# Performance work log

Measured on AMD Instinct MI355X. Metric: run time of the kernel, lower is better.

## Reference

```python
import jax, jax.numpy as jnp
import numpy as np

N = 100000      # nodes
E = 1600000     # edges (before self-loops)
IN_C = 128
HID = 256
L = 4
EPS = 1e-5


def setup_inputs() -> dict:
    key = jax.random.key(0)
    ks = jax.random.split(key, 12)
    s = 0.05
    x = jax.random.normal(ks[0], (N, IN_C), dtype=jnp.float32)
    edge_index = jax.random.randint(ks[1], (2, E), 0, N, dtype=jnp.int64)
    enc_w = jax.random.normal(ks[2], (IN_C, HID), dtype=jnp.float32) * s
    enc_b = jnp.zeros((HID,), jnp.float32)
    conv_w = jax.random.normal(ks[3], (L, HID, HID), dtype=jnp.float32) * s
    conv_b = jnp.zeros((L, HID), jnp.float32)
    ln_g = jnp.ones((L, HID), jnp.float32)
    ln_b = jnp.zeros((L, HID), jnp.float32)
    lin1_w = jax.random.normal(ks[4], (HID, HID // 2), dtype=jnp.float32) * s
    lin1_b = jnp.zeros((HID // 2,), jnp.float32)
    lin2_w = jax.random.normal(ks[5], (HID // 2, 1), dtype=jnp.float32) * s
    lin2_b = jnp.zeros((1,), jnp.float32)
    return dict(x=x, edge_index=edge_index, enc_w=enc_w, enc_b=enc_b,
                conv_w=conv_w, conv_b=conv_b, ln_g=ln_g, ln_b=ln_b,
                lin1_w=lin1_w, lin1_b=lin1_b, lin2_w=lin2_w, lin2_b=lin2_b)


def _layer_norm(h, g, b):
    mu = jnp.mean(h, axis=-1, keepdims=True)
    var = jnp.mean(jnp.square(h - mu), axis=-1, keepdims=True)
    return (h - mu) * jax.lax.rsqrt(var + EPS) * g + b


def reference(x, edge_index, enc_w, enc_b, conv_w, conv_b, ln_g, ln_b,
              lin1_w, lin1_b, lin2_w, lin2_b):
    loops = jnp.arange(N, dtype=edge_index.dtype)
    row = jnp.concatenate([edge_index[0], loops])   # source
    col = jnp.concatenate([edge_index[1], loops])   # target
    # GCN symmetric norm with self-loop weight 1 (improved=False)
    deg = jax.ops.segment_sum(jnp.ones(row.shape[0], jnp.float32), col,
                              num_segments=N)
    dis = jnp.where(deg > 0, jax.lax.rsqrt(deg), 0.0)  # deg^-1/2, [N]

    h = x @ enc_w + enc_b
    for i in range(L):
        hw = h @ conv_w[i]
        # norm_e = dis[row]*dis[col]: scale at source, aggregate, scale at target
        agg = jax.ops.segment_sum((hw * dis[:, None])[row], col,
                                  num_segments=N)
        h = agg * dis[:, None] + conv_b[i]
        h = jax.nn.relu(_layer_norm(h, ln_g[i], ln_b[i]))
        # dropout p=0.1 is identity in eval mode
    h = jax.nn.relu(h @ lin1_w + lin1_b)
    return h @ lin2_w + lin2_b  # [N, 1]
```

## Files before the change

kernel.cpp:

```cpp
#include <hip/hip_runtime.h>

#define N_NODES 100000
#define N_EDGES 1600000
#define IN_C    128
#define HID     256
#define NLAYER  4

#define NBUCK 391
#define BCAP  8192
#define EPB   4096
#define CAPL  6144

typedef __attribute__((ext_vector_type(8))) __bf16 bf16x8;
typedef __attribute__((ext_vector_type(4))) float  floatx4;

__device__ inline unsigned short f2b(float f) {
    unsigned u = __builtin_bit_cast(unsigned, f);
    return (unsigned short)((u + 0x7fffu + ((u >> 16) & 1u)) >> 16);
}
__device__ inline void acc8(float* a, uint4 v) {
    unsigned wds[4] = {v.x, v.y, v.z, v.w};
    #pragma unroll
    for (int k = 0; k < 4; ++k) {
        a[2*k]   += __builtin_bit_cast(float, wds[k] << 16);
        a[2*k+1] += __builtin_bit_cast(float, wds[k] & 0xffff0000u);
    }
}
__device__ inline void gl16(const void* g, void* l) {
    __builtin_amdgcn_global_load_lds(
        (const __attribute__((address_space(1))) unsigned int*)g,
        (__attribute__((address_space(3))) unsigned int*)l, 16, 0, 0);
}

__global__ __launch_bounds__(256) void kb_scatter(
        const int* __restrict__ row, const int* __restrict__ col,
        int* __restrict__ gfill, uint2* __restrict__ pairs, int e) {
    __shared__ uint2 ep[EPB];
    __shared__ int hist[NBUCK];
    __shared__ int lbase[NBUCK];
    const int tid  = threadIdx.x;
    const int base = blockIdx.x * EPB;
    for (int b = tid; b < NBUCK; b += 256) hist[b] = 0;
    __syncthreads();
    #pragma unroll
    for (int k = 0; k < EPB / 256; ++k) {
        int i = base + k * 256 + tid;
        uint2 pr = make_uint2(0xffffffffu, 0u);
        if (i < e) {
            pr.x = (unsigned)col[i];
            pr.y = (unsigned)row[i];
            atomicAdd(&hist[pr.x >> 8], 1);
        }
        ep[k * 256 + tid] = pr;
    }
    __syncthreads();
    for (int b = tid; b < NBUCK; b += 256) {
        int h = hist[b];
        lbase[b] = h ? atomicAdd(&gfill[b], h) : 0;
    }
    __syncthreads();
    for (int b = tid; b < NBUCK; b += 256) hist[b] = 0;
    __syncthreads();
    #pragma unroll
    for (int k = 0; k < EPB / 256; ++k) {
        uint2 pr = ep[k * 256 + tid];
        if (pr.x != 0xffffffffu) {
            int bk = pr.x >> 8;
            int p  = lbase[bk] + atomicAdd(&hist[bk], 1);
            if (p < BCAP) pairs[(size_t)bk * BCAP + p] = pr;
        }
    }
}

__global__ void kb_scan(const int* __restrict__ gfill, int* __restrict__ boff,
                        int* __restrict__ offs) {
    __shared__ int wsum[8];
    const int t = threadIdx.x, lane = t & 63, w = t >> 6;
    int v = (t < NBUCK) ? gfill[t] : 0;
    int inc = v;
    #pragma unroll
    for (int o = 1; o < 64; o <<= 1) { int u = __shfl_up(inc, o); if (lane >= o) inc += u; }
    if (lane == 63) wsum[w] = inc;
    __syncthreads();
    if (t == 0) { int r = 0; for (int i = 0; i < 8; ++i) { int x = wsum[i]; wsum[i] = r; r += x; } }
    __syncthreads();
    int excl = wsum[w] + inc - v;
    if (t <= NBUCK) boff[t] = excl;
    if (t == 0) offs[N_NODES] = N_EDGES;
}

__global__ __launch_bounds__(256) void kb_build(
        const uint2* __restrict__ pairs, const int* __restrict__ gfill,
        const int* __restrict__ boff,
        int* __restrict__ offs, float* __restrict__ dis,
        int* __restrict__ srcl, int n) {
    __shared__ int lcnt[256];
    __shared__ int lstart[256];
    __shared__ int wsum[4];
    __shared__ int sl[CAPL];
    const int b = blockIdx.x;
    const int tid = threadIdx.x, lane = tid & 63, w = tid >> 6;
    int cnt = gfill[b]; if (cnt > CAPL) cnt = CAPL;
    const int base = boff[b];
    const uint2* bp = pairs + (size_t)b * BCAP;
    lcnt[tid] = 0;
    __syncthreads();
    for (int i = tid; i < cnt; i += 256)
        atomicAdd(&lcnt[bp[i].x & 255], 1);
    __syncthreads();
    int v = lcnt[tid];
    int inc = v;
    #pragma unroll
    for (int o = 1; o < 64; o <<= 1) { int u = __shfl_up(inc, o); if (lane >= o) inc += u; }
    if (lane == 63) wsum[w] = inc;
    __syncthreads();
    if (tid == 0) { int r = 0; for (int i = 0; i < 4; ++i) { int x = wsum[i]; wsum[i] = r; r += x; } }
    __syncthreads();
    int excl = wsum[w] + inc - v;
    lstart[tid] = excl;
    int node = (b << 8) + tid;
    if (node < n) {
        dis[node]  = rsqrtf((float)(v + 1));
        offs[node] = base + excl;
    }
    __syncthreads();
    lcnt[tid] = 0;
    __syncthreads();
    for (int i = tid; i < cnt; i += 256) {
        uint2 pr = bp[i];
        int c = pr.x & 255;
        int q = lstart[c] + atomicAdd(&lcnt[c], 1);
        sl[q] = (int)pr.y;
    }
    __syncthreads();
    for (int i = tid; i < cnt; i += 256)
        srcl[base + i] = sl[i];
}

__global__ void k_wtz(const float* __restrict__ enc_w, const float* __restrict__ conv_w,
                      const float* __restrict__ w1,
                      unsigned short* __restrict__ enc_t, unsigned short* __restrict__ conv_t,
                      unsigned short* __restrict__ lin1_t, int* __restrict__ gfill) {
    int idx = blockIdx.x * blockDim.x + threadIdx.x;
    if (idx < NBUCK) gfill[idx] = 0;
    if (idx < IN_C * HID) {
        int k = idx / HID, n = idx % HID;
        enc_t[n * IN_C + k] = f2b(enc_w[idx]);
    } else if (idx < IN_C * HID + NLAYER * HID * HID) {
        int r = idx - IN_C * HID;
        int l = r / (HID * HID);
        int e = r % (HID * HID);
        int k = e / HID, n = e % HID;
        conv_t[(size_t)l * HID * HID + n * HID + k] = f2b(conv_w[r]);
    } else if (idx < IN_C * HID + NLAYER * HID * HID + HID * (HID / 2)) {
        int e = idx - (IN_C * HID + NLAYER * HID * HID);
        int k = e / (HID / 2), n = e % (HID / 2);
        lin1_t[n * HID + k] = f2b(w1[e]);
    }
}

__global__ __launch_bounds__(256) void k_mme(
        const float* __restrict__ Af,
        const unsigned short* __restrict__ Wt,
        const float* __restrict__ bias,
        unsigned short* __restrict__ Cout, int M) {
    const int K = IN_C, Nn = HID;
    __shared__ unsigned short As[128 * 32];
    __shared__ unsigned short Bs[128 * 32];
    const int tid  = threadIdx.x;
    const int lane = tid & 63;
    const int w    = tid >> 6;
    const int bm   = blockIdx.x * 128;
    const int bn   = blockIdx.y * 128;

    const int i0 = tid, i1 = tid + 256;
    const int r0 = i0 >> 2, r1 = i1 >> 2;
    const int q0 = i0 & 3,  q1 = i1 & 3;
    const int a_off0 = min(bm + r0, M - 1) * K + q0 * 8;
    const int a_off1 = min(bm + r1, M - 1) * K + q1 * 8;
    const int b_off0 = (bn + r0) * K + q0 * 8;
    const int b_off1 = (bn + r1) * K + q1 * 8;

    floatx4 acc[4][4];
    #pragma unroll
    for (int i = 0; i < 4; ++i)
        #pragma unroll
        for (int j = 0; j < 4; ++j)
            acc[i][j] = (floatx4){0.f, 0.f, 0.f, 0.f};

    const int wm = (w & 1) * 64;
    const int wn = (w >> 1) * 64;
    const int fm = lane & 15;
    const int fq = (lane >> 4) * 8;

    uint4 ra0, ra1, rb0, rb1;
    auto loadA = [&](int koff, uint4& oa0, uint4& oa1) {
        float4 f0 = *(const float4*)(Af + a_off0 + koff);
        float4 f1 = *(const float4*)(Af + a_off0 + koff + 4);
        oa0.x = (unsigned)f2b(f0.x) | ((unsigned)f2b(f0.y) << 16);
        oa0.y = (unsigned)f2b(f0.z) | ((unsigned)f2b(f0.w) << 16);
        oa0.z = (unsigned)f2b(f1.x) | ((unsigned)f2b(f1.y) << 16);
        oa0.w = (unsigned)f2b(f1.z) | ((unsigned)f2b(f1.w) << 16);
        float4 g0 = *(const float4*)(Af + a_off1 + koff);
        float4 g1 = *(const float4*)(Af + a_off1 + koff + 4);
        oa1.x = (unsigned)f2b(g0.x) | ((unsigned)f2b(g0.y) << 16);
        oa1.y = (unsigned)f2b(g0.z) | ((unsigned)f2b(g0.w) << 16);
        oa1.z = (unsigned)f2b(g1.x) | ((unsigned)f2b(g1.y) << 16);
        oa1.w = (unsigned)f2b(g1.z) | ((unsigned)f2b(g1.w) << 16);
    };

    loadA(0, ra0, ra1);
    rb0 = *(const uint4*)(Wt + b_off0);
    rb1 = *(const uint4*)(Wt + b_off1);

    const int KT = K >> 5;
    for (int kt = 0; kt < KT; ++kt) {
        ((uint4*)As)[i0] = ra0; ((uint4*)As)[i1] = ra1;
        ((uint4*)Bs)[i0] = rb0; ((uint4*)Bs)[i1] = rb1;
        __syncthreads();
        if (kt + 1 < KT) {
            int k0 = (kt + 1) << 5;
            loadA(k0, ra0, ra1);
            rb0 = *(const uint4*)(Wt + b_off0 + k0);
            rb1 = *(const uint4*)(Wt + b_off1 + k0);
        }
        bf16x8 af[4], bfr[4];
        #pragma unroll
        for (int i = 0; i < 4; ++i)
            af[i] = *(const bf16x8*)(const void*)(As + (wm + i * 16 + fm) * 32 + fq);
        #pragma unroll
        for (int j = 0; j < 4; ++j)
            bfr[j] = *(const bf16x8*)(const void*)(Bs + (wn + j * 16 + fm) * 32 + fq);
        #pragma unroll
        for (int i = 0; i < 4; ++i)
            #pragma unroll
            for (int j = 0; j < 4; ++j)
                acc[i][j] = __builtin_amdgcn_mfma_f32_16x16x32_bf16(af[i], bfr[j], acc[i][j], 0, 0, 0);
        __syncthreads();
    }

    const int quad = lane >> 4;
    #pragma unroll
    for (int i = 0; i < 4; ++i) {
        #pragma unroll
        for (int r = 0; r < 4; ++r) {
            int row = bm + wm + i * 16 + quad * 4 + r;
            if (row >= M) continue;
            #pragma unroll
            for (int j = 0; j < 4; ++j) {
                int colg = bn + wn + j * 16 + fm;
                float v = acc[i][j][r] + bias[colg];
                Cout[(size_t)row * Nn + colg] = f2b(v);
            }
        }
    }
}

__global__ __launch_bounds__(256) void k_mmc(
        const unsigned short* __restrict__ A,
        const unsigned short* __restrict__ Wt,
        const float* __restrict__ scale,
        unsigned short* __restrict__ Cout, int M) {
    const int K = HID, Nn = HID;
    __shared__ unsigned short As[128 * 32];
    __shared__ unsigned short Bs[128 * 32];
    const int tid  = threadIdx.x;
    const int lane = tid & 63;
    const int w    = tid >> 6;
    const int bm   = blockIdx.x * 128;
    const int bn   = blockIdx.y * 128;

    const int i0 = tid, i1 = tid + 256;
    const int r0 = i0 >> 2, r1 = i1 >> 2;
    const int q0 = i0 & 3,  q1 = i1 & 3;
    const int a_off0 = min(bm + r0, M - 1) * K + q0 * 8;
    const int a_off1 = min(bm + r1, M - 1) * K + q1 * 8;
    const int b_off0 = (bn + r0) * K + q0 * 8;
    const int b_off1 = (bn + r1) * K + q1 * 8;

    floatx4 acc[4][4];
    #pragma unroll
    for (int i = 0; i < 4; ++i)
        #pragma unroll
        for (int j = 0; j < 4; ++j)
            acc[i][j] = (floatx4){0.f, 0.f, 0.f, 0.f};

    const int wm = (w & 1) * 64;
    const int wn = (w >> 1) * 64;
    const int fm = lane & 15;
    const int fq = (lane >> 4) * 8;

    for (int kt = 0; kt < 8; ++kt) {
        int k0 = kt << 5;
        gl16(A  + a_off0 + k0, As + (size_t)i0 * 8);
        gl16(A  + a_off1 + k0, As + (size_t)i1 * 8);
        gl16(Wt + b_off0 + k0, Bs + (size_t)i0 * 8);
        gl16(Wt + b_off1 + k0, Bs + (size_t)i1 * 8);
        __syncthreads();
        bf16x8 af[4], bfr[4];
        #pragma unroll
        for (int i = 0; i < 4; ++i)
            af[i] = *(const bf16x8*)(const void*)(As + (wm + i * 16 + fm) * 32 + fq);
        #pragma unroll
        for (int j = 0; j < 4; ++j)
            bfr[j] = *(const bf16x8*)(const void*)(Bs + (wn + j * 16 + fm) * 32 + fq);
        #pragma unroll
        for (int i = 0; i < 4; ++i)
            #pragma unroll
            for (int j = 0; j < 4; ++j)
                acc[i][j] = __builtin_amdgcn_mfma_f32_16x16x32_bf16(af[i], bfr[j], acc[i][j], 0, 0, 0);
        __syncthreads();
    }

    const int quad = lane >> 4;
    #pragma unroll
    for (int i = 0; i < 4; ++i) {
        #pragma unroll
        for (int r = 0; r < 4; ++r) {
            int row = bm + wm + i * 16 + quad * 4 + r;
            if (row >= M) continue;
            float sc = scale[row];
            #pragma unroll
            for (int j = 0; j < 4; ++j) {
                int colg = bn + wn + j * 16 + fm;
                Cout[(size_t)row * Nn + colg] = f2b(acc[i][j][r] * sc);
            }
        }
    }
}

__global__ __launch_bounds__(256) void k_head(
        const unsigned short* __restrict__ A,
        const unsigned short* __restrict__ Wt,
        const float* __restrict__ b1, const float* __restrict__ w2,
        const float* __restrict__ b2, float* __restrict__ out, int M) {
    const int K = 256;
    __shared__ unsigned short As[128 * 32];
    __shared__ unsigned short Bs[128 * 32];
    const int tid  = threadIdx.x;
    const int lane = tid & 63;
    const int w    = tid >> 6;
    const int bm   = blockIdx.x * 128;

    const int i0 = tid, i1 = tid + 256;
    const int r0 = i0 >> 2, r1 = i1 >> 2;
    const int q0 = i0 & 3,  q1 = i1 & 3;
    const int a_off0 = min(bm + r0, M - 1) * K + q0 * 8;
    const int a_off1 = min(bm + r1, M - 1) * K + q1 * 8;
    const int b_off0 = r0 * K + q0 * 8;
    const int b_off1 = r1 * K + q1 * 8;

    floatx4 acc[4][4];
    #pragma unroll
    for (int i = 0; i < 4; ++i)
        #pragma unroll
        for (int j = 0; j < 4; ++j)
            acc[i][j] = (floatx4){0.f, 0.f, 0.f, 0.f};

    const int wm = (w & 1) * 64;
    const int wn = (w >> 1) * 64;
    const int fm = lane & 15;
    const int fq = (lane >> 4) * 8;

    for (int kt = 0; kt < 8; ++kt) {
        int k0 = kt << 5;
        gl16(A  + a_off0 + k0, As + (size_t)i0 * 8);
        gl16(A  + a_off1 + k0, As + (size_t)i1 * 8);
        gl16(Wt + b_off0 + k0, Bs + (size_t)i0 * 8);
        gl16(Wt + b_off1 + k0, Bs + (size_t)i1 * 8);
        __syncthreads();
        bf16x8 af[4], bfr[4];
        #pragma unroll
        for (int i = 0; i < 4; ++i)
            af[i] = *(const bf16x8*)(const void*)(As + (wm + i * 16 + fm) * 32 + fq);
        #pragma unroll
        for (int j = 0; j < 4; ++j)
            bfr[j] = *(const bf16x8*)(const void*)(Bs + (wn + j * 16 + fm) * 32 + fq);
        #pragma unroll
        for (int i = 0; i < 4; ++i)
            #pragma unroll
            for (int j = 0; j < 4; ++j)
                acc[i][j] = __builtin_amdgcn_mfma_f32_16x16x32_bf16(af[i], bfr[j], acc[i][j], 0, 0, 0);
        __syncthreads();
    }

    float* red = (float*)As;
    const int q = lane >> 4;
    float b1v[4], w2v[4];
    #pragma unroll
    for (int j = 0; j < 4; ++j) {
        int col = wn + j * 16 + fm;
        b1v[j] = b1[col]; w2v[j] = w2[col];
    }
    #pragma unroll
    for (int i = 0; i < 4; ++i) {
        #pragma unroll
        for (int r = 0; r < 4; ++r) {
            float s = 0.f;
            #pragma unroll
            for (int j = 0; j < 4; ++j)
                s += fmaxf(acc[i][j][r] + b1v[j], 0.f) * w2v[j];
            #pragma unroll
            for (int off = 1; off < 16; off <<= 1) s += __shfl_xor(s, off);
            if (fm == 0) {
                int m = wm + i * 16 + q * 4 + r;
                red[m * 2 + (wn >> 6)] = s;
            }
        }
    }
    __syncthreads();
    if (tid < 128) {
        int row = bm + tid;
        if (row < M) out[row] = red[tid * 2] + red[tid * 2 + 1] + b2[0];
    }
}

__global__ void k_agg(const unsigned short* __restrict__ hw, const int* __restrict__ srcl,
                      const int* __restrict__ offs, const float* __restrict__ dis,
                      const float* __restrict__ cb, const float* __restrict__ g,
                      const float* __restrict__ bt, unsigned short* __restrict__ hout, int n) {
    int gtid = blockIdx.x * blockDim.x + threadIdx.x;
    int node = __builtin_amdgcn_readfirstlane(gtid >> 6);
    int lane = threadIdx.x & 63;
    const int half = lane >> 5;
    const int sub  = lane & 31;
    const uint4* T = (const uint4*)hw;

    float a[8] = {0,0,0,0,0,0,0,0};
    float c[8] = {0,0,0,0,0,0,0,0};
    if (half == 0) {
        uint4 v = T[(size_t)node * 32 + sub];
        acc8(a, v);
    }
    int p = offs[node], pe = offs[node + 1];
    for (; p + 7 < pe; p += 8) {
        int s0 = srcl[p],     s1 = srcl[p + 1], s2 = srcl[p + 2], s3 = srcl[p + 3];
        int s4 = srcl[p + 4], s5 = srcl[p + 5], s6 = srcl[p + 6], s7 = srcl[p + 7];
        int ea = half ? s1 : s0;
        int eb = half ? s3 : s2;
        int ec = half ? s5 : s4;
        int ed = half ? s7 : s6;
        uint4 va = T[(size_t)ea * 32 + sub];
        uint4 vb = T[(size_t)eb * 32 + sub];
        uint4 vc = T[(size_t)ec * 32 + sub];
        uint4 vd = T[(size_t)ed * 32 + sub];
        acc8(a, va);
        acc8(c, vb);
        acc8(a, vc);
        acc8(c, vd);
    }
    for (; p + 1 < pe; p += 2) {
        int s0 = srcl[p], s1 = srcl[p + 1];
        int ea = half ? s1 : s0;
        uint4 v = T[(size_t)ea * 32 + sub];
        acc8(a, v);
    }
    if (p < pe && half == 0) {
        int s0 = srcl[p];
        uint4 v = T[(size_t)s0 * 32 + sub];
        acc8(a, v);
    }
    #pragma unroll
    for (int j = 0; j < 8; ++j) {
        a[j] += c[j];
        a[j] += __shfl_xor(a[j], 32);
    }
    float dc = dis[node];
    const float4* cb4 = (const float4*)cb;
    const float4* g4  = (const float4*)g;
    const float4* bt4 = (const float4*)bt;
    float4 cba = cb4[sub * 2], cbb = cb4[sub * 2 + 1];
    float h[8];
    h[0] = fmaf(a[0], dc, cba.x); h[1] = fmaf(a[1], dc, cba.y);
    h[2] = fmaf(a[2], dc, cba.z); h[3] = fmaf(a[3], dc, cba.w);
    h[4] = fmaf(a[4], dc, cbb.x); h[5] = fmaf(a[5], dc, cbb.y);
    h[6] = fmaf(a[6], dc, cbb.z); h[7] = fmaf(a[7], dc, cbb.w);
    float s = 0.f, sq = 0.f;
    #pragma unroll
    for (int j = 0; j < 8; ++j) { s += h[j]; sq += h[j] * h[j]; }
    #pragma unroll
    for (int off = 1; off < 32; off <<= 1) { s += __shfl_xor(s, off); sq += __shfl_xor(sq, off); }
    float mu  = s * (1.f / 256.f);
    float var = sq * (1.f / 256.f) - mu * mu;
    float inv = rsqrtf(var + 1e-5f);
    if (half == 0) {
        float4 ga = g4[sub * 2], gb = g4[sub * 2 + 1];
        float4 ba = bt4[sub * 2], bb = bt4[sub * 2 + 1];
        float gv[8] = {ga.x, ga.y, ga.z, ga.w, gb.x, gb.y, gb.z, gb.w};
        float bv[8] = {ba.x, ba.y, ba.z, ba.w, bb.x, bb.y, bb.z, bb.w};
        unsigned short o[8];
        #pragma unroll
        for (int j = 0; j < 8; ++j)
            o[j] = f2b(fmaxf(fmaf((h[j] - mu) * inv, gv[j], bv[j]), 0.f));
        uint4 st;
        st.x = (unsigned)o[0] | ((unsigned)o[1] << 16);
        st.y = (unsigned)o[2] | ((unsigned)o[3] << 16);
        st.z = (unsigned)o[4] | ((unsigned)o[5] << 16);
        st.w = (unsigned)o[6] | ((unsigned)o[7] << 16);
        ((uint4*)hout)[(size_t)node * 32 + sub] = st;
    }
}

extern "C" void kernel_launch(void* const* d_in, const int* in_sizes, int n_in,
                              void* d_out, int out_size, void* d_ws, size_t ws_size,
                              hipStream_t stream) {
    const float* x      = (const float*)d_in[0];
    const int*   ei     = (const int*)d_in[1];
    const float* enc_w  = (const float*)d_in[2];
    const float* enc_b  = (const float*)d_in[3];
    const float* conv_w = (const float*)d_in[4];
    const float* conv_b = (const float*)d_in[5];
    const float* ln_g   = (const float*)d_in[6];
    const float* ln_b   = (const float*)d_in[7];
    const float* w1     = (const float*)d_in[8];
    const float* b1     = (const float*)d_in[9];
    const float* w2     = (const float*)d_in[10];
    const float* b2     = (const float*)d_in[11];
    float* out = (float*)d_out;

    char* ws = (char*)d_ws;
    size_t off = 0;
    auto alloc = [&](size_t bytes) -> void* {
        void* p = ws + off;
        off = (off + bytes + 255) & ~(size_t)255;
        return p;
    };
    int*   offs  = (int*)alloc((size_t)(N_NODES + 1) * 4);
    int*   srcl  = (int*)alloc((size_t)N_EDGES * 4);
    float* dis   = (float*)alloc((size_t)N_NODES * 4);
    int*   gfill = (int*)alloc((size_t)NBUCK * 4);
    int*   boff  = (int*)alloc((size_t)(NBUCK + 1) * 4);
    unsigned short* hb = (unsigned short*)alloc((size_t)N_NODES * HID * 2);
    unsigned short* hw = (unsigned short*)alloc((size_t)N_NODES * HID * 2);
    uint2* pairs = (uint2*)alloc((size_t)NBUCK * BCAP * 8);
    unsigned short* enc_t  = (unsigned short*)alloc((size_t)IN_C * HID * 2);
    unsigned short* conv_t = (unsigned short*)alloc((size_t)NLAYER * HID * HID * 2);
    unsigned short* lin1_t = (unsigned short*)alloc((size_t)HID * (HID / 2) * 2);

    const int* row = ei;
    const int* col = ei + N_EDGES;

    {
        int tot = IN_C * HID + NLAYER * HID * HID + HID * (HID / 2);
        k_wtz<<<(tot + 255) / 256, 256, 0, stream>>>(enc_w, conv_w, w1,
                                                     enc_t, conv_t, lin1_t, gfill);
    }
    kb_scatter<<<(N_EDGES + EPB - 1) / EPB, 256, 0, stream>>>(row, col, gfill, pairs, N_EDGES);
    kb_scan<<<1, 512, 0, stream>>>(gfill, boff, offs);
    kb_build<<<NBUCK, 256, 0, stream>>>(pairs, gfill, boff, offs, dis, srcl, N_NODES);

    {
        dim3 g((N_NODES + 127) / 128, HID / 128);
        k_mme<<<g, 256, 0, stream>>>(x, enc_t, enc_b, hb, N_NODES);
    }

    for (int l = 0; l < NLAYER; ++l) {
        dim3 g((N_NODES + 127) / 128, HID / 128);
        k_mmc<<<g, 256, 0, stream>>>(hb, conv_t + (size_t)l * HID * HID, dis, hw, N_NODES);
        k_agg<<<(N_NODES * 64 + 255) / 256, 256, 0, stream>>>(
            hw, srcl, offs, dis, conv_b + l * HID, ln_g + l * HID, ln_b + l * HID, hb, N_NODES);
    }

    k_head<<<(N_NODES + 127) / 128, 256, 0, stream>>>(hb, lin1_t, b1, w2, b2, out, N_NODES);
}
```

Baseline: 800.9 us.

## Widen GEMM tiles to full 256-column output with 512-thread blocks

The encoder and per-layer conv GEMMs now compute all 256 output columns per block using 8 waves, instead of two column blocks of 128. Each A row tile is loaded (and, for the fp32 encoder, converted to bf16) once rather than twice, halving A reads and block count. The encoder also switches its B loads to direct async global-to-LDS copies instead of register staging. Costs are larger LDS per block and fewer, larger blocks, which may reduce occupancy or latency hiding.

After: 779.8 us (median of 2 runs). -2.6%, faster.

```diff
diff --git a/kernel.cpp b/kernel.cpp
--- a/kernel.cpp
+++ b/kernel.cpp
@@ -159,27 +159,23 @@
     }
 }
 
-__global__ __launch_bounds__(256) void k_mme(
+__global__ __launch_bounds__(512) void k_mme(
         const float* __restrict__ Af,
         const unsigned short* __restrict__ Wt,
         const float* __restrict__ bias,
         unsigned short* __restrict__ Cout, int M) {
-    const int K = IN_C, Nn = HID;
+    const int K = IN_C;
     __shared__ unsigned short As[128 * 32];
-    __shared__ unsigned short Bs[128 * 32];
+    __shared__ unsigned short Bs[256 * 32];
     const int tid  = threadIdx.x;
     const int lane = tid & 63;
     const int w    = tid >> 6;
     const int bm   = blockIdx.x * 128;
-    const int bn   = blockIdx.y * 128;
-
-    const int i0 = tid, i1 = tid + 256;
-    const int r0 = i0 >> 2, r1 = i1 >> 2;
-    const int q0 = i0 & 3,  q1 = i1 & 3;
-    const int a_off0 = min(bm + r0, M - 1) * K + q0 * 8;
-    const int a_off1 = min(bm + r1, M - 1) * K + q1 * 8;
-    const int b_off0 = (bn + r0) * K + q0 * 8;
-    const int b_off1 = (bn + r1) * K + q1 * 8;
+
+    const int r0 = tid >> 2, q0 = tid & 3;
+    const int a_off  = min(bm + r0, M - 1) * K + q0 * 8;
+    const int b_off0 = r0 * K + q0 * 8;
+    const int b_off1 = (r0 + 128) * K + q0 * 8;
 
     floatx4 acc[4][4];
     #pragma unroll
@@ -193,37 +189,26 @@
     const int fm = lane & 15;
     const int fq = (lane >> 4) * 8;
 
-    uint4 ra0, ra1, rb0, rb1;
-    auto loadA = [&](int koff, uint4& oa0, uint4& oa1) {
-        float4 f0 = *(const float4*)(Af + a_off0 + koff);
-        float4 f1 = *(const float4*)(Af + a_off0 + koff + 4);
-        oa0.x = (unsigned)f2b(f0.x) | ((unsigned)f2b(f0.y) << 16);
-        oa0.y = (unsigned)f2b(f0.z) | ((unsigned)f2b(f0.w) << 16);
-        oa0.z = (unsigned)f2b(f1.x) | ((unsigned)f2b(f1.y) << 16);
-        oa0.w = (unsigned)f2b(f1.z) | ((unsigned)f2b(f1.w) << 16);
-        float4 g0 = *(const float4*)(Af + a_off1 + koff);
-        float4 g1 = *(const float4*)(Af + a_off1 + koff + 4);
-        oa1.x = (unsigned)f2b(g0.x) | ((unsigned)f2b(g0.y) << 16);
-        oa1.y = (unsigned)f2b(g0.z) | ((unsigned)f2b(g0.w) << 16);
-        oa1.z = (unsigned)f2b(g1.x) | ((unsigned)f2b(g1.y) << 16);
-        oa1.w = (unsigned)f2b(g1.z) | ((unsigned)f2b(g1.w) << 16);
+    uint4 ra;
+    auto loadA = [&](int koff, uint4& oa) {
+        float4 f0 = *(const float4*)(Af + a_off + koff);
+        float4 f1 = *(const float4*)(Af + a_off + koff + 4);
+        oa.x = (unsigned)f2b(f0.x) | ((unsigned)f2b(f0.y) << 16);
+        oa.y = (unsigned)f2b(f0.z) | ((unsigned)f2b(f0.w) << 16);
+        oa.z = (unsigned)f2b(f1.x) | ((unsigned)f2b(f1.y) << 16);
+        oa.w = (unsigned)f2b(f1.z) | ((unsigned)f2b(f1.w) << 16);
     };
 
-    loadA(0, ra0, ra1);
-    rb0 = *(const uint4*)(Wt + b_off0);
-    rb1 = *(const uint4*)(Wt + b_off1);
+    loadA(0, ra);
 
     const int KT = K >> 5;
     for (int kt = 0; kt < KT; ++kt) {
-        ((uint4*)As)[i0] = ra0; ((uint4*)As)[i1] = ra1;
-        ((uint4*)Bs)[i0] = rb0; ((uint4*)Bs)[i1] = rb1;
+        int k0 = kt << 5;
+        ((uint4*)As)[tid] = ra;
+        gl16(Wt + b_off0 + k0, Bs + (size_t)tid * 8);
+        gl16(Wt + b_off1 + k0, Bs + (size_t)(tid + 512) * 8);
         __syncthreads();
-        if (kt + 1 < KT) {
-            int k0 = (kt + 1) << 5;
-            loadA(k0, ra0, ra1);
-            rb0 = *(const uint4*)(Wt + b_off0 + k0);
-            rb1 = *(const uint4*)(Wt + b_off1 + k0);
-        }
+        if (kt + 1 < KT) loadA((kt + 1) << 5, ra);
         bf16x8 af[4], bfr[4];
         #pragma unroll
         for (int i = 0; i < 4; ++i)
@@ -248,35 +233,31 @@
             if (row >= M) continue;
             #pragma unroll
             for (int j = 0; j < 4; ++j) {
-                int colg = bn + wn + j * 16 + fm;
+                int colg = wn + j * 16 + fm;
                 float v = acc[i][j][r] + bias[colg];
-                Cout[(size_t)row * Nn + colg] = f2b(v);
+                Cout[(size_t)row * HID + colg] = f2b(v);
             }
         }
     }
 }
 
-__global__ __launch_bounds__(256) void k_mmc(
+__global__ __launch_bounds__(512) void k_mmc(
         const unsigned short* __restrict__ A,
         const unsigned short* __restrict__ Wt,
         const float* __restrict__ scale,
         unsigned short* __restrict__ Cout, int M) {
-    const int K = HID, Nn = HID;
+    const int K = HID;
     __shared__ unsigned short As[128 * 32];
-    __shared__ unsigned short Bs[128 * 32];
+    __shared__ unsigned short Bs[256 * 32];
     const int tid  = threadIdx.x;
     const int lane = tid & 63;
     const int w    = tid >> 6;
     const int bm   = blockIdx.x * 128;
-    const int bn   = blockIdx.y * 128;
-
-    const int i0 = tid, i1 = tid + 256;
-    const int r0 = i0 >> 2, r1 = i1 >> 2;
-    const int q0 = i0 & 3,  q1 = i1 & 3;
-    const int a_off0 = min(bm + r0, M - 1) * K + q0 * 8;
-    const int a_off1 = min(bm + r1, M - 1) * K + q1 * 8;
-    const int b_off0 = (bn + r0) * K + q0 * 8;
-    const int b_off1 = (bn + r1) * K + q1 * 8;
+
+    const int r0 = tid >> 2, q0 = tid & 3;
+    const int a_off  = min(bm + r0, M - 1) * K + q0 * 8;
+    const int b_off0 = r0 * K + q0 * 8;
+    const int b_off1 = (r0 + 128) * K + q0 * 8;
 
     floatx4 acc[4][4];
     #pragma unroll
@@ -292,10 +273,9 @@
 
     for (int kt = 0; kt < 8; ++kt) {
         int k0 = kt << 5;
-        gl16(A  + a_off0 + k0, As + (size_t)i0 * 8);
-        gl16(A  + a_off1 + k0, As + (size_t)i1 * 8);
-        gl16(Wt + b_off0 + k0, Bs + (size_t)i0 * 8);
-        gl16(Wt + b_off1 + k0, Bs + (size_t)i1 * 8);
+        gl16(A  + a_off  + k0, As + (size_t)tid * 8);
+        gl16(Wt + b_off0 + k0, Bs + (size_t)tid * 8);
+        gl16(Wt + b_off1 + k0, Bs + (size_t)(tid + 512) * 8);
         __syncthreads();
         bf16x8 af[4], bfr[4];
         #pragma unroll
@@ -322,8 +302,8 @@
             float sc = scale[row];
             #pragma unroll
             for (int j = 0; j < 4; ++j) {
-                int colg = bn + wn + j * 16 + fm;
-                Cout[(size_t)row * Nn + colg] = f2b(acc[i][j][r] * sc);
+                int colg = wn + j * 16 + fm;
+                Cout[(size_t)row * HID + colg] = f2b(acc[i][j][r] * sc);
             }
         }
     }
@@ -549,14 +529,11 @@
     kb_scan<<<1, 512, 0, stream>>>(gfill, boff, offs);
     kb_build<<<NBUCK, 256, 0, stream>>>(pairs, gfill, boff, offs, dis, srcl, N_NODES);
 
-    {
-        dim3 g((N_NODES + 127) / 128, HID / 128);
-        k_mme<<<g, 256, 0, stream>>>(x, enc_t, enc_b, hb, N_NODES);
-    }
+    k_mme<<<(N_NODES + 127) / 128, 512, 0, stream>>>(x, enc_t, enc_b, hb, N_NODES);
 
     for (int l = 0; l < NLAYER; ++l) {
-        dim3 g((N_NODES + 127) / 128, HID / 128);
-        k_mmc<<<g, 256, 0, stream>>>(hb, conv_t + (size_t)l * HID * HID, dis, hw, N_NODES);
+        k_mmc<<<(N_NODES + 127) / 128, 512, 0, stream>>>(
+            hb, conv_t + (size_t)l * HID * HID, dis, hw, N_NODES);
         k_agg<<<(N_NODES * 64 + 255) / 256, 256, 0, stream>>>(
             hw, srcl, offs, dis, conv_b + l * HID, ln_g + l * HID, ln_b + l * HID, hb, N_NODES);
     }
```
